# Performance work log

Hardware: AMD Instinct MI355X
Metric: run time of the kernel (lower is better)

The kernel has to match this reference:

```python
import jax, jax.numpy as jnp
import numpy as np

BETA = 0.25


def setup_inputs() -> dict:
    key = jax.random.key(0)
    k1, k2 = jax.random.split(key)
    z = jax.random.normal(k1, (8, 256, 16, 16, 16), dtype=jnp.float32)
    n_codes, dim = 2048, 256
    # original init: uniform(-1/n_codes, 1/n_codes)
    emb = jax.random.uniform(k2, (n_codes, dim), dtype=jnp.float32,
                             minval=-1.0 / n_codes, maxval=1.0 / n_codes)
    return {"z": z, "emb": emb}


def reference(z, emb):
    B, C, D, H, W = z.shape  # C == embedding_dim
    # channels-last flatten: [B*D*H*W, C]
    z_flat = jnp.transpose(z, (0, 2, 3, 4, 1)).reshape(-1, C)
    # squared L2 distances to each code: [N, K]
    dist = (jnp.sum(z_flat * z_flat, axis=1, keepdims=True)
            + jnp.sum(emb * emb, axis=1)
            - 2.0 * jnp.dot(z_flat, emb.T))
    idx = jnp.argmin(dist, axis=1)  # [N] int
    # FAITHFUL to original: gathered codes are reshaped directly to z.shape
    # (B, C, D, H, W) WITHOUT undoing the channels-last permute.
    z_q = jnp.take(emb, idx, axis=0).reshape(z.shape)
    commitment_loss = jnp.mean((jax.lax.stop_gradient(z_q) - z) ** 2)
    codebook_loss = jnp.mean((z_q - jax.lax.stop_gradient(z)) ** 2)
    vq_loss = codebook_loss + BETA * commitment_loss
    z_q_st = z + jax.lax.stop_gradient(z_q - z)  # straight-through
    return (z_q_st, vq_loss, idx)
```

## Files before the change

kernel.cpp:

```cpp
#include <hip/hip_runtime.h>
#include <float.h>

#define N_PTS    32768
#define N_CODES  2048
#define DIM      256
#define S_STRIDE 4096
#define B_STRIDE 1048576
#define N_ELEM   8388608

#define MARGIN   8e-4f

#define WS_PARTIAL 0
#define WS_E2      512
#define WS_EB      8704
#define WS_ZT      1057280
#define WS_TMIN    17834496
#define WS_STATS   34611712
#define WS_EMBP    WS_ZT

typedef unsigned short ushort_t;
typedef short bf16x8 __attribute__((ext_vector_type(8)));
typedef float f32x4 __attribute__((ext_vector_type(4)));

__device__ __forceinline__ ushort_t f2bf(float v) {
    const unsigned u = __float_as_uint(v);
    return (ushort_t)((u + 0x7FFFu + ((u >> 16) & 1u)) >> 16);
}

__device__ __forceinline__ void async_copy16(void* lds, const void* g) {
    __builtin_amdgcn_global_load_lds(
        (const __attribute__((address_space(1))) unsigned int*)g,
        (__attribute__((address_space(3))) unsigned int*)lds, 16, 0, 0);
}

__device__ __forceinline__ void nt_store4(float* p, f32x4 v) {
    __builtin_nontemporal_store(v, reinterpret_cast<f32x4*>(p));
}

__global__ void conv_emb_kernel(const float* __restrict__ emb, ushort_t* __restrict__ eb) {
    const int gid = blockIdx.x * 256 + threadIdx.x;
    const int k = gid >> 6, c4 = gid & 63;
    const float4 u = *reinterpret_cast<const float4*>(emb + (size_t)k * DIM + c4 * 4);
    ushort4 v; v.x = f2bf(u.x); v.y = f2bf(u.y); v.z = f2bf(u.z); v.w = f2bf(u.w);
    *reinterpret_cast<ushort4*>(eb + (size_t)k * DIM + c4 * 4) = v;
}

__global__ void perm_emb_kernel(const float* __restrict__ emb, float* __restrict__ embp) {
    const int gid = blockIdx.x * 256 + threadIdx.x;
    const int ql = gid & 15, c4 = (gid >> 4) & 63, g = gid >> 10;
    const float4 u = reinterpret_cast<const float4*>(emb)[(size_t)(g * 16 + ql) * 64 + c4];
    reinterpret_cast<float4*>(embp)[gid] = u;
}

__global__ void e2p_kernel(const float* __restrict__ emb, float* __restrict__ e2,
                           float* __restrict__ partial) {
    const int k = blockIdx.x * 256 + threadIdx.x;
    if (blockIdx.x == 0 && threadIdx.x < 64) partial[threadIdx.x] = 0.f;
    const float* base = emb + (size_t)k * DIM;
    float half[2];
    #pragma unroll
    for (int h = 0; h < 2; ++h) {
        float r[8];
        #pragma unroll
        for (int j = 0; j < 8; ++j) { const float v = base[h * 128 + j]; r[j] = __fmul_rn(v, v); }
        for (int t = 8; t < 128; t += 8)
            #pragma unroll
            for (int j = 0; j < 8; ++j) {
                const float v = base[h * 128 + t + j];
                r[j] = __fadd_rn(r[j], __fmul_rn(v, v));
            }
        half[h] = __fadd_rn(__fadd_rn(__fadd_rn(r[0], r[1]), __fadd_rn(r[2], r[3])),
                            __fadd_rn(__fadd_rn(r[4], r[5]), __fadd_rn(r[6], r[7])));
    }
    e2[k] = __fadd_rn(half[0], half[1]);
}

__global__ void transpose_kernel(const float* __restrict__ z, ushort_t* __restrict__ zt) {
    __shared__ ushort_t lt[64][72];
    const int bx = blockIdx.x;
    const int b = bx >> 8, cg = (bx >> 6) & 3, sg = bx & 63;
    const int c0 = cg * 64, s0 = sg * 64;
    const int t = threadIdx.x;
    {
        const int cl = t >> 4, s4 = t & 15;
        #pragma unroll
        for (int j = 0; j < 4; ++j) {
            const int c = cl + 16 * j;
            const float4 u = *reinterpret_cast<const float4*>(
                z + (size_t)b * B_STRIDE + (size_t)(c0 + c) * S_STRIDE + s0 + s4 * 4);
            ushort4 v; v.x = f2bf(u.x); v.y = f2bf(u.y); v.z = f2bf(u.z); v.w = f2bf(u.w);
            *reinterpret_cast<ushort4*>(&lt[c][s4 * 4]) = v;
        }
    }
    __syncthreads();
    {
        const int sl = t >> 4, c4 = t & 15;
        #pragma unroll
        for (int j = 0; j < 4; ++j) {
            const int s = sl + 16 * j;
            ushort4 v;
            v.x = lt[c4 * 4 + 0][s]; v.y = lt[c4 * 4 + 1][s];
            v.z = lt[c4 * 4 + 2][s]; v.w = lt[c4 * 4 + 3][s];
            *reinterpret_cast<ushort4*>(zt + (size_t)(b * 4096 + s0 + s) * DIM + c0 + c4 * 4) = v;
        }
    }
}

__global__ __launch_bounds__(256, 4) void screen_kernel(
    const ushort_t* __restrict__ zt, const ushort_t* __restrict__ eb,
    const float* __restrict__ e2, float* __restrict__ tmin,
    float* __restrict__ stats)
{
    __shared__ char lds[32768];
    __shared__ float e2s[128];
    const int tid = threadIdx.x;
    const int x = blockIdx.x;
    const int bm = (x & 7) * 32 + ((x >> 3) & 31), bn = x >> 8;
    const int n0 = bm * 128, k0 = bn * 128;
    if (tid < 128) e2s[tid] = e2[k0 + tid];
    const int wv = tid >> 6, lane = tid & 63;
    const int col = lane & 15, quad = lane >> 4;
    const int pcr = quad ^ ((col >> 1) & 3);

    f32x4 acc[2][8];
    #pragma unroll
    for (int j = 0; j < 2; ++j)
        #pragma unroll
        for (int i = 0; i < 8; ++i) acc[j][i] = (f32x4){0.f, 0.f, 0.f, 0.f};

    #define STAGE(kc_, half_)                                                       \
        {                                                                           \
            const int base_ = (half_) * 16384;                                      \
            _Pragma("unroll")                                                       \
            for (int it = 0; it < 4; ++it) {                                        \
                const int L = tid + it * 256;                                       \
                if (L < 512) {                                                      \
                    const int row = L >> 2, pc = L & 3, c = pc ^ ((row >> 1) & 3);  \
                    async_copy16(lds + base_ + L * 16,                              \
                                 zt + ((size_t)(n0 + row) * DIM + (kc_) * 32 + c * 8)); \
                } else {                                                            \
                    const int L2 = L - 512;                                         \
                    const int row = L2 >> 2, pc = L2 & 3, c = pc ^ ((row >> 1) & 3);\
                    async_copy16(lds + base_ + 8192 + L2 * 16,                      \
                                 eb + ((size_t)(k0 + row) * DIM + (kc_) * 32 + c * 8)); \
                }                                                                   \
            }                                                                       \
        }

    STAGE(0, 0);
    __syncthreads();
    #pragma unroll
    for (int kc = 0; kc < 8; ++kc) {
        const int cur = kc & 1;
        if (kc < 7) STAGE(kc + 1, cur ^ 1);
        {
            const char* zb = lds + cur * 16384;
            const char* ebb = zb + 8192;
            bf16x8 af[2];
            #pragma unroll
            for (int j = 0; j < 2; ++j) {
                const int crow = wv * 32 + j * 16 + col;
                af[j] = *reinterpret_cast<const bf16x8*>(ebb + (crow * 4 + pcr) * 16);
            }
            #pragma unroll
            for (int i = 0; i < 8; ++i) {
                const int prow = i * 16 + col;
                const bf16x8 bq = *reinterpret_cast<const bf16x8*>(zb + (prow * 4 + pcr) * 16);
                #pragma unroll
                for (int j = 0; j < 2; ++j)
                    acc[j][i] = __builtin_amdgcn_mfma_f32_16x16x32_bf16(af[j], bq, acc[j][i], 0, 0, 0);
            }
        }
        __syncthreads();
    }
    #undef STAGE

    float* res  = reinterpret_cast<float*>(lds);
    float* sbuf = reinterpret_cast<float*>(lds + 8192);
    float ej[2][4];
    #pragma unroll
    for (int j = 0; j < 2; ++j) {
        const f32x4 e4 = *reinterpret_cast<const f32x4*>(&e2s[wv * 32 + j * 16 + quad * 4]);
        ej[j][0] = e4[0]; ej[j][1] = e4[1]; ej[j][2] = e4[2]; ej[j][3] = e4[3];
    }
    #pragma unroll
    for (int j = 0; j < 2; ++j) {
        #pragma unroll
        for (int i = 0; i < 8; ++i) {
            float tm[4];
            #pragma unroll
            for (int r = 0; r < 4; ++r) tm[r] = fmaf(-2.f, acc[j][i][r], ej[j][r]);
            float m = fminf(fminf(tm[0], tm[1]), fminf(tm[2], tm[3]));
            m = fminf(m, __shfl_xor(m, 16));
            m = fminf(m, __shfl_xor(m, 32));
            if (quad == 0)
                res[(i * 16 + col) * 12 + wv * 2 + j] = m;
        }
    }
    #pragma unroll
    for (int i = 0; i < 8; ++i) {
        float m1 = FLT_MAX, m2 = FLT_MAX; int i1 = 0;
        #pragma unroll
        for (int j = 0; j < 2; ++j) {
            #pragma unroll
            for (int r = 0; r < 4; ++r) {
                const float v = fmaf(-2.f, acc[j][i][r], ej[j][r]);
                const int idx = k0 + wv * 32 + j * 16 + quad * 4 + r;
                if (v < m1) { m2 = m1; m1 = v; i1 = idx; }
                else if (v < m2) { m2 = v; }
            }
        }
        #pragma unroll
        for (int off = 16; off <= 32; off <<= 1) {
            const float om1 = __shfl_xor(m1, off);
            const float om2 = __shfl_xor(m2, off);
            const int   oi1 = __shfl_xor(i1, off);
            if (om1 < m1) { m2 = fminf(om2, m1); m1 = om1; i1 = oi1; }
            else          { m2 = fminf(m2, om1); }
        }
        if (quad == 0) {
            const int p = i * 16 + col;
            sbuf[p * 12 + wv * 3 + 0] = m1;
            sbuf[p * 12 + wv * 3 + 1] = (float)i1;
            sbuf[p * 12 + wv * 3 + 2] = m2;
        }
    }
    __syncthreads();
    {
        const int p = tid >> 1, h = tid & 1;
        const f32x4 v = *reinterpret_cast<const f32x4*>(&res[p * 12 + h * 4]);
        *reinterpret_cast<f32x4*>(
            &tmin[((size_t)bn * N_PTS + n0 + p) * 8 + h * 4]) = v;
    }
    if (tid < 128) {
        const int p = tid;
        float m1 = sbuf[p * 12 + 0], i1 = sbuf[p * 12 + 1], m2 = sbuf[p * 12 + 2];
        #pragma unroll
        for (int w = 1; w < 4; ++w) {
            const float bm1 = sbuf[p * 12 + w * 3 + 0];
            const float bi1 = sbuf[p * 12 + w * 3 + 1];
            const float bm2 = sbuf[p * 12 + w * 3 + 2];
            if (bm1 < m1) { m2 = fminf(m1, bm2); m1 = bm1; i1 = bi1; }
            else          { m2 = fminf(m2, bm1); }
        }
        f32x4 st; st[0] = m1; st[1] = i1; st[2] = m2; st[3] = 0.f;
        *reinterpret_cast<f32x4*>(&stats[((size_t)bn * N_PTS + n0 + p) * 4]) = st;
    }
}

__global__ __launch_bounds__(256, 3) void exact_kernel(
    const float* __restrict__ z, const float* __restrict__ emb,
    const float* __restrict__ embp,
    const float* __restrict__ e2, const float* __restrict__ tmin,
    const float* __restrict__ stats,
    float* __restrict__ outf, float* __restrict__ out_idx, float* __restrict__ partial)
{
    __shared__ float zs[32 * 260];
    const int tid = threadIdx.x;
    const int n0 = blockIdx.x * 32;
    const int b = n0 >> 12, s0 = n0 & 4095;
    {
        const int tq = tid & 7, cg = tid >> 3;
        for (int c = cg; c < DIM; c += 32) {
            const float4 u = *reinterpret_cast<const float4*>(
                z + (size_t)b * B_STRIDE + (size_t)c * S_STRIDE + s0 + tq * 4);
            zs[(tq * 4 + 0) * 260 + c] = u.x;
            zs[(tq * 4 + 1) * 260 + c] = u.y;
            zs[(tq * 4 + 2) * 260 + c] = u.z;
            zs[(tq * 4 + 3) * 260 + c] = u.w;
        }
    }
    __syncthreads();
    const int wv = tid >> 6, lane = tid & 63;
    const int quad = lane >> 4, ql = lane & 15;
    float lossacc = 0.f;

    float a[2][8]; f32x4 st[2];
    #pragma unroll
    for (int t = 0; t < 2; ++t) {
        const int n = n0 + wv * 8 + t * 4 + quad;
        #pragma unroll
        for (int i = 0; i < 8; ++i)
            a[t][i] = __builtin_nontemporal_load(
                tmin + ((size_t)(i * 2 + (ql >> 3)) * N_PTS + n) * 8 + (ql & 7));
        st[t] = *reinterpret_cast<const f32x4*>(&stats[((size_t)ql * N_PTS + n) * 4]);
    }

    #pragma unroll
    for (int t = 0; t < 2; ++t) {
        const int p = wv * 8 + t * 4 + quad;
        const int n = n0 + p;
        const float* zr = &zs[p * 260];
        float m1 = st[t][0], i1f = st[t][1], m2 = st[t][2];
        #pragma unroll
        for (int off = 1; off < 16; off <<= 1) {
            const float om1 = __shfl_xor(m1, off);
            const float oi1 = __shfl_xor(i1f, off);
            const float om2 = __shfl_xor(m2, off);
            if (om1 < m1) { m2 = fminf(m1, om2); m1 = om1; i1f = oi1; }
            else          { m2 = fminf(m2, om1); }
        }
        const bool shortcut = (m2 - m1 > MARGIN);
        float bs = FLT_MAX; int bkf = 0x7FFFFFFF;
        if (!shortcut) {
            const int h = ql >> 3, j = ql & 7;
            float v0 = zr[h * 128 + j];
            float r = __fmul_rn(v0, v0);
            #pragma unroll
            for (int t2 = 1; t2 < 16; ++t2) {
                const float v = zr[h * 128 + j + 8 * t2];
                r = __fadd_rn(r, __fmul_rn(v, v));
            }
            { float v = __shfl_xor(r, 1); r = __fadd_rn(r, v); }
            { float v = __shfl_xor(r, 2); r = __fadd_rn(r, v); }
            { float v = __shfl_xor(r, 4); r = __fadd_rn(r, v); }
            const float z2n = __fadd_rn(__shfl(r, quad * 16), __shfl(r, quad * 16 + 8));
            float mn = fminf(fminf(fminf(a[t][0], a[t][1]), fminf(a[t][2], a[t][3])),
                             fminf(fminf(a[t][4], a[t][5]), fminf(a[t][6], a[t][7])));
            #pragma unroll
            for (int off = 1; off < 16; off <<= 1) mn = fminf(mn, __shfl_xor(mn, off));
            const float thr = mn + MARGIN;
            unsigned long long M0 = 0ull, M1 = 0ull;
            #pragma unroll
            for (int i = 0; i < 8; ++i) {
                const unsigned long long bal = __ballot(a[t][i] <= thr);
                const unsigned long long bits = (bal >> (quad * 16)) & 0xFFFFull;
                if (i < 4) M0 |= bits << (i * 16);
                else       M1 |= bits << ((i - 4) * 16);
            }
            while (__any((M0 | M1) != 0ull)) {
                int myt = -1;
                if (M0) { myt = __ffsll(M0) - 1; M0 &= M0 - 1; }
                else if (M1) { myt = 64 + __ffsll(M1) - 1; M1 &= M1 - 1; }
                if (myt >= 0) {
                    const int kg = myt * 16 + ql;
                    const float e2k = e2[kg];
                    const float4* gp = reinterpret_cast<const float4*>(embp)
                                       + (size_t)myt * 1024 + ql;
                    float4 pre[8];
                    #pragma unroll
                    for (int s8 = 0; s8 < 8; ++s8) pre[s8] = gp[s8 * 16];
                    float dot = 0.f;
                    #pragma unroll
                    for (int seg = 0; seg < 8; ++seg) {
                        float4 cur[8];
                        #pragma unroll
                        for (int s8 = 0; s8 < 8; ++s8) cur[s8] = pre[s8];
                        if (seg < 7) {
                            #pragma unroll
                            for (int s8 = 0; s8 < 8; ++s8)
                                pre[s8] = gp[(seg + 1) * 128 + s8 * 16];
                        }
                        #pragma unroll
                        for (int s8 = 0; s8 < 8; ++s8) {
                            const int c4 = seg * 8 + s8;
                            const float4 zv = *reinterpret_cast<const float4*>(zr + c4 * 4);
                            dot = fmaf(zv.x, cur[s8].x, dot);
                            dot = fmaf(zv.y, cur[s8].y, dot);
                            dot = fmaf(zv.z, cur[s8].z, dot);
                            dot = fmaf(zv.w, cur[s8].w, dot);
                        }
                    }
                    const float A = __fadd_rn(z2n, e2k);
                    const float s = __fsub_rn(A, __fmul_rn(2.f, dot));
                    if (s < bs || (s == bs && kg < bkf)) { bs = s; bkf = kg; }
                }
            }
            #pragma unroll
            for (int off = 1; off < 16; off <<= 1) {
                const float os = __shfl_xor(bs, off);
                const int ok = __shfl_xor(bkf, off);
                if (os < bs || (os == bs && ok < bkf)) { bs = os; bkf = ok; }
            }
        }
        const int bk = shortcut ? (int)i1f : bkf;
        const float* eq = emb + (size_t)bk * DIM;
        float* op = outf + (size_t)n * DIM;
        #pragma unroll
        for (int jj = 0; jj < 4; ++jj) {
            const int c = (jj * 16 + ql) * 4;
            const float4 q4 = *reinterpret_cast<const float4*>(eq + c);
            f32x4 q; q[0] = q4.x; q[1] = q4.y; q[2] = q4.z; q[3] = q4.w;
            nt_store4(op + c, q);
            float d;
            d = q4.x - zr[c + 0]; lossacc = fmaf(d, d, lossacc);
            d = q4.y - zr[c + 1]; lossacc = fmaf(d, d, lossacc);
            d = q4.z - zr[c + 2]; lossacc = fmaf(d, d, lossacc);
            d = q4.w - zr[c + 3]; lossacc = fmaf(d, d, lossacc);
        }
        if (ql == 0) out_idx[n] = (float)bk;
    }
    #pragma unroll
    for (int off = 1; off < 64; off <<= 1) lossacc += __shfl_xor(lossacc, off);
    if (lane == 0) atomicAdd(&partial[blockIdx.x & 63], lossacc);
}

__global__ void finalize_kernel(const float* __restrict__ partial, float* __restrict__ out_loss) {
    float v = partial[threadIdx.x];
    #pragma unroll
    for (int off = 1; off < 64; off <<= 1) v += __shfl_xor(v, off);
    if (threadIdx.x == 0)
        *out_loss = v * 1.25f / (float)N_ELEM;
}

extern "C" void kernel_launch(void* const* d_in, const int* in_sizes, int n_in,
                              void* d_out, int out_size, void* d_ws, size_t ws_size,
                              hipStream_t stream) {
    const float* z = (const float*)d_in[0];
    const float* emb = (const float*)d_in[1];
    char* ws = (char*)d_ws;
    float* partial = (float*)(ws + WS_PARTIAL);
    float* e2 = (float*)(ws + WS_E2);
    ushort_t* eb = (ushort_t*)(ws + WS_EB);
    ushort_t* zt = (ushort_t*)(ws + WS_ZT);
    float* embp = (float*)(ws + WS_EMBP);
    float* tmin = (float*)(ws + WS_TMIN);
    float* stats = (float*)(ws + WS_STATS);
    float* outf = (float*)d_out;
    float* out_loss = outf + N_ELEM;
    float* out_idx = outf + N_ELEM + 1;

    conv_emb_kernel<<<512, 256, 0, stream>>>(emb, eb);
    e2p_kernel<<<N_CODES / 256, 256, 0, stream>>>(emb, e2, partial);
    transpose_kernel<<<2048, 256, 0, stream>>>(z, zt);
    screen_kernel<<<4096, 256, 0, stream>>>(zt, eb, e2, tmin, stats);
    perm_emb_kernel<<<512, 256, 0, stream>>>(emb, embp);
    exact_kernel<<<N_PTS / 32, 256, 0, stream>>>(z, emb, embp, e2, tmin, stats,
                                                 outf, out_idx, partial);
    finalize_kernel<<<1, 64, 0, stream>>>(partial, out_loss);
}
```

Baseline: 232.0 us.

## Compact fallback rescoring across quads and load tmin only for ambiguous points

Points that need exact fallback rescoring are first gathered into a per-wave bitmask. They are then processed four at a time, one per 16-lane quad, so divergent quads no longer idle while one quad rescans candidate codes. Shortcut points gather their codes right away, and the tmin candidate tiles are now loaded only for points that need fallback, which cuts memory traffic. The cost is a separate loop with more control overhead, and the tmin loads are no longer issued up front where their latency was hidden.

After: 233.5 us. No clear change (+0.7%).

```diff
diff --git a/kernel.cpp b/kernel.cpp
--- a/kernel.cpp
+++ b/kernel.cpp
@@ -275,23 +275,33 @@
     const int quad = lane >> 4, ql = lane & 15;
     float lossacc = 0.f;
 
-    float a[2][8]; f32x4 st[2];
-    #pragma unroll
-    for (int t = 0; t < 2; ++t) {
-        const int n = n0 + wv * 8 + t * 4 + quad;
-        #pragma unroll
-        for (int i = 0; i < 8; ++i)
-            a[t][i] = __builtin_nontemporal_load(
-                tmin + ((size_t)(i * 2 + (ql >> 3)) * N_PTS + n) * 8 + (ql & 7));
-        st[t] = *reinterpret_cast<const f32x4*>(&stats[((size_t)ql * N_PTS + n) * 4]);
-    }
-
+#define GATHER(bk_, n_, zr_)                                                   \
+    {                                                                          \
+        const float* eq = emb + (size_t)(bk_) * DIM;                           \
+        float* op = outf + (size_t)(n_) * DIM;                                 \
+        _Pragma("unroll")                                                      \
+        for (int jj = 0; jj < 4; ++jj) {                                       \
+            const int c = (jj * 16 + ql) * 4;                                  \
+            const float4 q4 = *reinterpret_cast<const float4*>(eq + c);        \
+            f32x4 q; q[0] = q4.x; q[1] = q4.y; q[2] = q4.z; q[3] = q4.w;       \
+            nt_store4(op + c, q);                                              \
+            float d;                                                           \
+            d = q4.x - (zr_)[c + 0]; lossacc = fmaf(d, d, lossacc);            \
+            d = q4.y - (zr_)[c + 1]; lossacc = fmaf(d, d, lossacc);            \
+            d = q4.z - (zr_)[c + 2]; lossacc = fmaf(d, d, lossacc);            \
+            d = q4.w - (zr_)[c + 3]; lossacc = fmaf(d, d, lossacc);            \
+        }                                                                      \
+        if (ql == 0) out_idx[n_] = (float)(bk_);                               \
+    }
+
+    int fb_mask = 0;
     #pragma unroll
     for (int t = 0; t < 2; ++t) {
         const int p = wv * 8 + t * 4 + quad;
         const int n = n0 + p;
-        const float* zr = &zs[p * 260];
-        float m1 = st[t][0], i1f = st[t][1], m2 = st[t][2];
+        const f32x4 st = *reinterpret_cast<const f32x4*>(
+            &stats[((size_t)ql * N_PTS + n) * 4]);
+        float m1 = st[0], i1f = st[1], m2 = st[2];
         #pragma unroll
         for (int off = 1; off < 16; off <<= 1) {
             const float om1 = __shfl_xor(m1, off);
@@ -301,8 +311,36 @@
             else          { m2 = fminf(m2, om1); }
         }
         const bool shortcut = (m2 - m1 > MARGIN);
-        float bs = FLT_MAX; int bkf = 0x7FFFFFFF;
-        if (!shortcut) {
+        const unsigned long long bal = __ballot(!shortcut);
+        const int bits4 = (int)(((bal >> 0) & 1) | (((bal >> 16) & 1) << 1) |
+                                (((bal >> 32) & 1) << 2) | (((bal >> 48) & 1) << 3));
+        fb_mask |= bits4 << (t * 4);
+        if (shortcut) {
+            const int bk = (int)i1f;
+            const float* zr = &zs[p * 260];
+            GATHER(bk, n, zr);
+        }
+    }
+
+    while (fb_mask) {
+        int sel[4];
+        #pragma unroll
+        for (int sl = 0; sl < 4; ++sl) {
+            int s = -1;
+            if (fb_mask) { s = __ffs(fb_mask) - 1; fb_mask &= fb_mask - 1; }
+            sel[sl] = s;
+        }
+        const int myslot = sel[quad];
+        const int p = wv * 8 + (myslot >= 0 ? myslot : 0);
+        const int n = n0 + p;
+        const float* zr = &zs[p * 260];
+        unsigned long long M0 = 0ull, M1 = 0ull;
+        float z2n = 0.f;
+        if (myslot >= 0) {
+            float a[8];
+            #pragma unroll
+            for (int i = 0; i < 8; ++i)
+                a[i] = tmin[((size_t)(i * 2 + (ql >> 3)) * N_PTS + n) * 8 + (ql & 7)];
             const int h = ql >> 3, j = ql & 7;
             float v0 = zr[h * 128 + j];
             float r = __fmul_rn(v0, v0);
@@ -314,82 +352,71 @@
             { float v = __shfl_xor(r, 1); r = __fadd_rn(r, v); }
             { float v = __shfl_xor(r, 2); r = __fadd_rn(r, v); }
             { float v = __shfl_xor(r, 4); r = __fadd_rn(r, v); }
-            const float z2n = __fadd_rn(__shfl(r, quad * 16), __shfl(r, quad * 16 + 8));
-            float mn = fminf(fminf(fminf(a[t][0], a[t][1]), fminf(a[t][2], a[t][3])),
-                             fminf(fminf(a[t][4], a[t][5]), fminf(a[t][6], a[t][7])));
+            z2n = __fadd_rn(__shfl(r, quad * 16), __shfl(r, quad * 16 + 8));
+            float mn = fminf(fminf(fminf(a[0], a[1]), fminf(a[2], a[3])),
+                             fminf(fminf(a[4], a[5]), fminf(a[6], a[7])));
             #pragma unroll
             for (int off = 1; off < 16; off <<= 1) mn = fminf(mn, __shfl_xor(mn, off));
             const float thr = mn + MARGIN;
-            unsigned long long M0 = 0ull, M1 = 0ull;
             #pragma unroll
             for (int i = 0; i < 8; ++i) {
-                const unsigned long long bal = __ballot(a[t][i] <= thr);
+                const unsigned long long bal = __ballot(a[i] <= thr);
                 const unsigned long long bits = (bal >> (quad * 16)) & 0xFFFFull;
                 if (i < 4) M0 |= bits << (i * 16);
                 else       M1 |= bits << ((i - 4) * 16);
             }
-            while (__any((M0 | M1) != 0ull)) {
-                int myt = -1;
-                if (M0) { myt = __ffsll(M0) - 1; M0 &= M0 - 1; }
-                else if (M1) { myt = 64 + __ffsll(M1) - 1; M1 &= M1 - 1; }
-                if (myt >= 0) {
-                    const int kg = myt * 16 + ql;
-                    const float e2k = e2[kg];
-                    const float4* gp = reinterpret_cast<const float4*>(embp)
-                                       + (size_t)myt * 1024 + ql;
-                    float4 pre[8];
+        }
+        float bs = FLT_MAX; int bkf = 0x7FFFFFFF;
+        while (__any((M0 | M1) != 0ull)) {
+            int myt = -1;
+            if (M0) { myt = __ffsll(M0) - 1; M0 &= M0 - 1; }
+            else if (M1) { myt = 64 + __ffsll(M1) - 1; M1 &= M1 - 1; }
+            if (myt >= 0) {
+                const int kg = myt * 16 + ql;
+                const float e2k = e2[kg];
+                const float4* gp = reinterpret_cast<const float4*>(embp)
+                                   + (size_t)myt * 1024 + ql;
+                float4 pre[8];
+                #pragma unroll
+                for (int s8 = 0; s8 < 8; ++s8) pre[s8] = gp[s8 * 16];
+                float dot = 0.f;
+                #pragma unroll
+                for (int seg = 0; seg < 8; ++seg) {
+                    float4 cur[8];
                     #pragma unroll
-                    for (int s8 = 0; s8 < 8; ++s8) pre[s8] = gp[s8 * 16];
-                    float dot = 0.f;
+                    for (int s8 = 0; s8 < 8; ++s8) cur[s8] = pre[s8];
+                    if (seg < 7) {
+                        #pragma unroll
+                        for (int s8 = 0; s8 < 8; ++s8)
+                            pre[s8] = gp[(seg + 1) * 128 + s8 * 16];
+                    }
                     #pragma unroll
-                    for (int seg = 0; seg < 8; ++seg) {
-                        float4 cur[8];
-                        #pragma unroll
-                        for (int s8 = 0; s8 < 8; ++s8) cur[s8] = pre[s8];
-                        if (seg < 7) {
-                            #pragma unroll
-                            for (int s8 = 0; s8 < 8; ++s8)
-                                pre[s8] = gp[(seg + 1) * 128 + s8 * 16];
-                        }
-                        #pragma unroll
-                        for (int s8 = 0; s8 < 8; ++s8) {
-                            const int c4 = seg * 8 + s8;
-                            const float4 zv = *reinterpret_cast<const float4*>(zr + c4 * 4);
-                            dot = fmaf(zv.x, cur[s8].x, dot);
-                            dot = fmaf(zv.y, cur[s8].y, dot);
-                            dot = fmaf(zv.z, cur[s8].z, dot);
-                            dot = fmaf(zv.w, cur[s8].w, dot);
-                        }
+                    for (int s8 = 0; s8 < 8; ++s8) {
+                        const int c4 = seg * 8 + s8;
+                        const float4 zv = *reinterpret_cast<const float4*>(zr + c4 * 4);
+                        dot = fmaf(zv.x, cur[s8].x, dot);
+                        dot = fmaf(zv.y, cur[s8].y, dot);
+                        dot = fmaf(zv.z, cur[s8].z, dot);
+                        dot = fmaf(zv.w, cur[s8].w, dot);
                     }
-                    const float A = __fadd_rn(z2n, e2k);
-                    const float s = __fsub_rn(A, __fmul_rn(2.f, dot));
-                    if (s < bs || (s == bs && kg < bkf)) { bs = s; bkf = kg; }
                 }
-            }
-            #pragma unroll
-            for (int off = 1; off < 16; off <<= 1) {
-                const float os = __shfl_xor(bs, off);
-                const int ok = __shfl_xor(bkf, off);
-                if (os < bs || (os == bs && ok < bkf)) { bs = os; bkf = ok; }
-            }
-        }
-        const int bk = shortcut ? (int)i1f : bkf;
-        const float* eq = emb + (size_t)bk * DIM;
-        float* op = outf + (size_t)n * DIM;
-        #pragma unroll
-        for (int jj = 0; jj < 4; ++jj) {
-            const int c = (jj * 16 + ql) * 4;
-            const float4 q4 = *reinterpret_cast<const float4*>(eq + c);
-            f32x4 q; q[0] = q4.x; q[1] = q4.y; q[2] = q4.z; q[3] = q4.w;
-            nt_store4(op + c, q);
-            float d;
-            d = q4.x - zr[c + 0]; lossacc = fmaf(d, d, lossacc);
-            d = q4.y - zr[c + 1]; lossacc = fmaf(d, d, lossacc);
-            d = q4.z - zr[c + 2]; lossacc = fmaf(d, d, lossacc);
-            d = q4.w - zr[c + 3]; lossacc = fmaf(d, d, lossacc);
-        }
-        if (ql == 0) out_idx[n] = (float)bk;
-    }
+                const float A = __fadd_rn(z2n, e2k);
+                const float s = __fsub_rn(A, __fmul_rn(2.f, dot));
+                if (s < bs || (s == bs && kg < bkf)) { bs = s; bkf = kg; }
+            }
+        }
+        #pragma unroll
+        for (int off = 1; off < 16; off <<= 1) {
+            const float os = __shfl_xor(bs, off);
+            const int ok = __shfl_xor(bkf, off);
+            if (os < bs || (os == bs && ok < bkf)) { bs = os; bkf = ok; }
+        }
+        if (myslot >= 0) {
+            GATHER(bkf, n, zr);
+        }
+    }
+    #undef GATHER
+
     #pragma unroll
     for (int off = 1; off < 64; off <<= 1) lossacc += __shfl_xor(lossacc, off);
     if (lane == 0) atomicAdd(&partial[blockIdx.x & 63], lossacc);
```
